# Kernel optimization log

Hardware: AMD Instinct MI355X
Metric: run time of the kernel (lower is better)

## Reference

```python
import jax, jax.numpy as jnp
import numpy as np

N, E, T = 50000, 800000, 3
FIN, H, D, FE = 256, 4, 64, 64
NEG_SLOPE = 0.2


def setup_inputs() -> dict:
    key = jax.random.key(0)
    ks = jax.random.split(key, 10)
    x = jax.random.normal(ks[0], (N, FIN), dtype=jnp.float32)
    edge_src = jax.random.randint(ks[1], (E,), 0, N, dtype=jnp.int32)
    edge_dst = jax.random.randint(ks[2], (E,), 0, N, dtype=jnp.int32)
    edge_type = jax.random.randint(ks[3], (E,), 0, T, dtype=jnp.int32)
    s = 1.0 / np.sqrt(FIN)
    W = jax.random.normal(ks[4], (FIN, H * D), dtype=jnp.float32) * s
    edge_emb = jax.random.normal(ks[5], (T, FE), dtype=jnp.float32)
    W_e = jax.random.normal(ks[6], (FE, H * FE), dtype=jnp.float32) * (1.0 / np.sqrt(FE))
    attn_l = jax.random.normal(ks[7], (H, D), dtype=jnp.float32) * (1.0 / np.sqrt(D))
    attn_r = jax.random.normal(ks[8], (H, D), dtype=jnp.float32) * (1.0 / np.sqrt(D))
    attn_e = jax.random.normal(ks[9], (H, FE), dtype=jnp.float32) * (1.0 / np.sqrt(FE))
    return {"x": x, "edge_src": edge_src, "edge_dst": edge_dst,
            "edge_type": edge_type, "W": W, "edge_emb": edge_emb,
            "W_e": W_e, "attn_l": attn_l, "attn_r": attn_r, "attn_e": attn_e}


def reference(x, edge_src, edge_dst, edge_type, W, edge_emb, W_e, attn_l, attn_r, attn_e):
    # node projection: [N, H, D]
    feat = (x @ W).reshape(N, H, D)
    # per-node, per-head attention scalars
    el = jnp.einsum('nhd,hd->nh', feat, attn_l)  # [N, H]
    er = jnp.einsum('nhd,hd->nh', feat, attn_r)  # [N, H]
    # per-edge-type attention scalar: edge_emb[t] @ W_e -> [T, H, FE]
    e_feat = (edge_emb @ W_e).reshape(T, H, FE)
    ee = jnp.einsum('the,he->th', e_feat, attn_e)  # [T, H]
    # per-edge logits, leaky-relu
    logits = jax.nn.leaky_relu(el[edge_src] + er[edge_dst] + ee[edge_type], NEG_SLOPE)  # [E, H]
    # edge softmax over incoming edges of each dst node (all etypes together)
    seg_max = jax.ops.segment_max(logits, edge_dst, num_segments=N)  # [N, H]
    seg_max = jnp.where(jnp.isfinite(seg_max), seg_max, 0.0)
    expl = jnp.exp(logits - seg_max[edge_dst])  # [E, H]
    seg_sum = jax.ops.segment_sum(expl, edge_dst, num_segments=N)  # [N, H]
    a = expl / seg_sum[edge_dst]  # [E, H]
    # weighted scatter-sum aggregation: sum over incoming edges
    msg = feat[edge_src] * a[:, :, None]  # [E, H, D]
    out = jax.ops.segment_sum(msg, edge_dst, num_segments=N)  # [N, H, D]
    return out, a
```

## Files before the change

### kernel.cpp

```cpp
#include <hip/hip_runtime.h>
#include <hip/hip_bf16.h>
#include <math.h>

#define N_NODES 50000
#define E_EDGES 800000
#define T_TYPES 3
#define MAXDEG 64
#define NEG_SLOPE 0.2f
#define GEMM_BLOCKS 782

typedef __attribute__((ext_vector_type(8))) short short8;
typedef __attribute__((ext_vector_type(4))) short short4v;
typedef __attribute__((ext_vector_type(4))) float f32x4;

__device__ inline short f2bf(float f) {
    __hip_bfloat16 h = __float2bfloat16(f);
    union { __hip_bfloat16 b; short s; } u;
    u.b = h;
    return u.s;
}
__device__ inline float bf2f(short s) {
    union { unsigned u; float f; } v;
    v.u = ((unsigned)(unsigned short)s) << 16;
    return v.f;
}

__global__ void k_prep(const float* __restrict__ W, short8* __restrict__ WF,
                       const float* __restrict__ edge_emb, const float* __restrict__ W_e,
                       const float* __restrict__ attn_e, float* __restrict__ ee,
                       unsigned* __restrict__ deg) {
    int b = blockIdx.x;
    if (b < 32) {
        int f = b * 256 + threadIdx.x;
        int lane = f & 63;
        int rest = f >> 6;
        int ks = rest & 7;
        int nfh = rest >> 3;
        int l15 = lane & 15;
        int lq = lane >> 4;
        int row = nfh * 16 + l15;
        int col0 = ks * 32 + lq * 8;
        short8 s;
        #pragma unroll
        for (int j = 0; j < 8; ++j)
            s[j] = f2bf(W[(size_t)(col0 + j) * 256 + row]);
        WF[f] = s;
    } else if (b < 32 + T_TYPES) {
        int t = b - 32;
        int j = threadIdx.x;
        int h = j >> 6;
        float ae = attn_e[j];
        float v = 0.f;
        #pragma unroll
        for (int k = 0; k < 64; ++k) v += edge_emb[t * 64 + k] * W_e[k * 256 + j];
        v *= ae;
        #pragma unroll
        for (int o = 32; o; o >>= 1) v += __shfl_xor(v, o, 64);
        if ((j & 63) == 0) ee[t * 4 + h] = v;
    } else {
        int i = (b - 32 - T_TYPES) * 256 + threadIdx.x;
        if (i < N_NODES) deg[i] = 0u;
    }
}

__global__ __launch_bounds__(256) void k_gs(const float* __restrict__ x, const short8* __restrict__ WF,
                                            const float* __restrict__ attn_l, const float* __restrict__ attn_r,
                                            short* __restrict__ featb, float* __restrict__ el,
                                            float* __restrict__ er,
                                            const int* __restrict__ esrc, const int* __restrict__ edst,
                                            const int* __restrict__ etype, unsigned* __restrict__ deg,
                                            unsigned* __restrict__ A) {
    __shared__ short lds[64][264];
    if (blockIdx.x >= GEMM_BLOCKS) {
        int e = (blockIdx.x - GEMM_BLOCKS) * 256 + threadIdx.x;
        if (e < E_EDGES) {
            int s = esrc[e], d = edst[e], t = etype[e];
            unsigned rank = atomicAdd(&deg[d], 1u);
            if (rank < MAXDEG)
                A[d * MAXDEG + rank] = (unsigned)s | ((unsigned)t << 16);
        }
        return;
    }

    const int tid = threadIdx.x;
    const int wc = tid >> 6;
    const int lane = tid & 63;
    const int l15 = lane & 15;
    const int lq = lane >> 4;
    const int m0 = blockIdx.x * 64;

    #pragma unroll
    for (int i = 0; i < 16; ++i) {
        int idx = tid + 256 * i;
        int r = idx >> 6;
        int c4 = idx & 63;
        int gr = m0 + r;
        if (gr >= N_NODES) gr = N_NODES - 1;
        float4 v = *reinterpret_cast<const float4*>(&x[(size_t)gr * 256 + c4 * 4]);
        short4v s;
        s[0] = f2bf(v.x); s[1] = f2bf(v.y); s[2] = f2bf(v.z); s[3] = f2bf(v.w);
        *reinterpret_cast<short4v*>(&lds[r][c4 * 4]) = s;
    }
    __syncthreads();

    const short8* wfbase = &WF[(size_t)(wc * 4) * 8 * 64 + lane];

    f32x4 acc[4][4];
    #pragma unroll
    for (int mf = 0; mf < 4; ++mf)
        #pragma unroll
        for (int nf = 0; nf < 4; ++nf)
            acc[mf][nf] = (f32x4){0.f, 0.f, 0.f, 0.f};

    #pragma unroll 2
    for (int k0 = 0; k0 < 256; k0 += 32) {
        const int ks = k0 >> 5;
        short8 av[4], bv[4];
        #pragma unroll
        for (int mf = 0; mf < 4; ++mf)
            av[mf] = *reinterpret_cast<const short8*>(&lds[mf * 16 + l15][k0 + lq * 8]);
        #pragma unroll
        for (int nf = 0; nf < 4; ++nf)
            bv[nf] = wfbase[(nf * 8 + ks) * 64];
        #pragma unroll
        for (int mf = 0; mf < 4; ++mf)
            #pragma unroll
            for (int nf = 0; nf < 4; ++nf)
                acc[mf][nf] = __builtin_amdgcn_mfma_f32_16x16x32_bf16(av[mf], bv[nf], acc[mf][nf], 0, 0, 0);
    }

    float al[4], ar[4];
    #pragma unroll
    for (int nf = 0; nf < 4; ++nf) {
        al[nf] = attn_l[wc * 64 + nf * 16 + l15];
        ar[nf] = attn_r[wc * 64 + nf * 16 + l15];
    }
    #pragma unroll
    for (int mf = 0; mf < 4; ++mf) {
        #pragma unroll
        for (int i = 0; i < 4; ++i) {
            int m = m0 + mf * 16 + lq * 4 + i;
            bool ok = m < N_NODES;
            float pl = 0.f, pr = 0.f;
            #pragma unroll
            for (int nf = 0; nf < 4; ++nf) {
                float v = acc[mf][nf][i];
                if (ok) featb[(size_t)m * 256 + wc * 64 + nf * 16 + l15] = f2bf(v);
                pl += v * al[nf];
                pr += v * ar[nf];
            }
            #pragma unroll
            for (int o = 1; o < 16; o <<= 1) {
                pl += __shfl_xor(pl, o, 64);
                pr += __shfl_xor(pr, o, 64);
            }
            if (ok && l15 == 0) {
                el[m * 4 + wc] = pl;
                er[m * 4 + wc] = pr;
            }
        }
    }
}

__global__ __launch_bounds__(256) void k_agg(const unsigned* __restrict__ deg, const unsigned* __restrict__ A,
                                             const float* __restrict__ el, const float* __restrict__ er,
                                             const float* __restrict__ ee, const short* __restrict__ featb,
                                             float* __restrict__ out, float* __restrict__ invp) {
    const int wave = threadIdx.x >> 6;
    const int lane = threadIdx.x & 63;
    const int n = blockIdx.x * 4 + wave;
    if (n >= N_NODES) return;
    const int half = lane >> 5;
    const int l32 = lane & 31;
    const int h = l32 >> 3;
    unsigned cnt = deg[n];
    if (cnt > MAXDEG) cnt = MAXDEG;
    const unsigned base = (unsigned)n * MAXDEG;

    const float ern = er[n * 4 + h];
    const float ee0 = ee[h], ee1 = ee[4 + h], ee2 = ee[8 + h];

    float s0 = 0.f, s1 = 0.f;
    float a0[8], a1[8];
    #pragma unroll
    for (int j = 0; j < 8; ++j) { a0[j] = 0.f; a1[j] = 0.f; }
    {
        unsigned i = half;
        for (; i + 2 < cnt; i += 4) {
            unsigned p0 = A[base + i];
            unsigned p1 = A[base + i + 2];
            unsigned src0 = p0 & 0xFFFFu, t0 = p0 >> 16;
            unsigned src1 = p1 & 0xFFFFu, t1 = p1 >> 16;
            float el0 = el[src0 * 4 + h];
            float el1 = el[src1 * 4 + h];
            short8 f0 = *reinterpret_cast<const short8*>(&featb[(size_t)src0 * 256 + l32 * 8]);
            short8 f1 = *reinterpret_cast<const short8*>(&featb[(size_t)src1 * 256 + l32 * 8]);
            float z0 = (el0 + ern) + (t0 == 0 ? ee0 : (t0 == 1 ? ee1 : ee2));
            float z1 = (el1 + ern) + (t1 == 0 ? ee0 : (t1 == 1 ? ee1 : ee2));
            z0 = z0 > 0.f ? z0 : NEG_SLOPE * z0;
            z1 = z1 > 0.f ? z1 : NEG_SLOPE * z1;
            float w0 = __expf(z0);
            float w1 = __expf(z1);
            s0 += w0; s1 += w1;
            #pragma unroll
            for (int j = 0; j < 8; ++j) {
                a0[j] += w0 * bf2f(f0[j]);
                a1[j] += w1 * bf2f(f1[j]);
            }
        }
        for (; i < cnt; i += 2) {
            unsigned p0 = A[base + i];
            unsigned src0 = p0 & 0xFFFFu, t0 = p0 >> 16;
            float el0 = el[src0 * 4 + h];
            short8 f0 = *reinterpret_cast<const short8*>(&featb[(size_t)src0 * 256 + l32 * 8]);
            float z0 = (el0 + ern) + (t0 == 0 ? ee0 : (t0 == 1 ? ee1 : ee2));
            z0 = z0 > 0.f ? z0 : NEG_SLOPE * z0;
            float w0 = __expf(z0);
            s0 += w0;
            #pragma unroll
            for (int j = 0; j < 8; ++j) a0[j] += w0 * bf2f(f0[j]);
        }
    }
    float s = s0 + s1;
    s += __shfl_xor(s, 32, 64);
    #pragma unroll
    for (int j = 0; j < 8; ++j) {
        a0[j] += a1[j];
        a0[j] += __shfl_xor(a0[j], 32, 64);
    }
    float inv = (cnt > 0) ? 1.f / s : 0.f;

    if (half == 0) {
        float4 o0, o1;
        o0.x = a0[0] * inv; o0.y = a0[1] * inv; o0.z = a0[2] * inv; o0.w = a0[3] * inv;
        o1.x = a0[4] * inv; o1.y = a0[5] * inv; o1.z = a0[6] * inv; o1.w = a0[7] * inv;
        *reinterpret_cast<float4*>(&out[(size_t)n * 256 + l32 * 8]) = o0;
        *reinterpret_cast<float4*>(&out[(size_t)n * 256 + l32 * 8 + 4]) = o1;
        if ((l32 & 7) == 0) invp[n * 4 + h] = inv;
    }
}

__global__ void k_edge(const int* __restrict__ esrc, const int* __restrict__ edst,
                       const int* __restrict__ etype, const float* __restrict__ el,
                       const float* __restrict__ er, const float* __restrict__ ee,
                       const float* __restrict__ invp, float* __restrict__ a_out) {
    int e = blockIdx.x * 256 + threadIdx.x;
    if (e >= E_EDGES) return;
    int s = esrc[e], d = edst[e], t = etype[e];
    float4 l = *reinterpret_cast<const float4*>(&el[s * 4]);
    float4 r = *reinterpret_cast<const float4*>(&er[d * 4]);
    float4 q = *reinterpret_cast<const float4*>(&ee[t * 4]);
    float4 iv = *reinterpret_cast<const float4*>(&invp[d * 4]);
    float4 z;
    z.x = (l.x + r.x) + q.x;
    z.y = (l.y + r.y) + q.y;
    z.z = (l.z + r.z) + q.z;
    z.w = (l.w + r.w) + q.w;
    z.x = z.x > 0.f ? z.x : NEG_SLOPE * z.x;
    z.y = z.y > 0.f ? z.y : NEG_SLOPE * z.y;
    z.z = z.z > 0.f ? z.z : NEG_SLOPE * z.z;
    z.w = z.w > 0.f ? z.w : NEG_SLOPE * z.w;
    float4 av;
    av.x = __expf(z.x) * iv.x;
    av.y = __expf(z.y) * iv.y;
    av.z = __expf(z.z) * iv.z;
    av.w = __expf(z.w) * iv.w;
    *reinterpret_cast<float4*>(&a_out[(size_t)e * 4]) = av;
}

extern "C" void kernel_launch(void* const* d_in, const int* in_sizes, int n_in,
                              void* d_out, int out_size, void* d_ws, size_t ws_size,
                              hipStream_t stream) {
    const float* x        = (const float*)d_in[0];
    const int*   edge_src = (const int*)d_in[1];
    const int*   edge_dst = (const int*)d_in[2];
    const int*   edge_type= (const int*)d_in[3];
    const float* W        = (const float*)d_in[4];
    const float* edge_emb = (const float*)d_in[5];
    const float* W_e      = (const float*)d_in[6];
    const float* attn_l   = (const float*)d_in[7];
    const float* attn_r   = (const float*)d_in[8];
    const float* attn_e   = (const float*)d_in[9];

    float* out   = (float*)d_out;
    float* a_out = (float*)d_out + (size_t)N_NODES * 256;

    char* ws = (char*)d_ws;
    short*    featb   = (short*)(ws + 0);
    float*    el      = (float*)(ws + 25600000);
    float*    er      = (float*)(ws + 26400000);
    float*    ee      = (float*)(ws + 27200000);
    unsigned* deg     = (unsigned*)(ws + 27200064);
    float*    invp    = (float*)(ws + 27400064);
    unsigned* A       = (unsigned*)(ws + 28200064);
    short8*   WF      = (short8*)(ws + 41000064);

    const int degBlocks = (N_NODES + 255) / 256;
    k_prep<<<32 + T_TYPES + degBlocks, 256, 0, stream>>>(W, WF, edge_emb, W_e, attn_e, ee, deg);

    const int scatterBlocks = (E_EDGES + 255) / 256;
    k_gs<<<GEMM_BLOCKS + scatterBlocks, 256, 0, stream>>>(x, WF, attn_l, attn_r, featb, el, er,
                                                          edge_src, edge_dst, edge_type, deg, A);

    k_agg<<<(N_NODES + 3) / 4, 256, 0, stream>>>(deg, A, el, er, ee, featb, out, invp);
    k_edge<<<(E_EDGES + 255) / 256, 256, 0, stream>>>(edge_src, edge_dst, edge_type,
                                                      el, er, ee, invp, a_out);
}
```

Baseline: 156.7 us.

## Shard per-node degree counters to reduce atomic contention in edge bucketing

Replaces the single per-destination atomic counter and 64-slot adjacency list with 8 shards per node (16 slots each), picking the shard from the edge index. This spreads same-address atomics across separate counters in the scatter phase. The aggregation kernel now reads 8 shard counts and walks two shard pairs per half-wave. In exchange the zero-init and adjacency buffers grow, aggregation does extra count loads and branchier indexing, and any shard holding more than 16 edges drops edges.

```diff
diff --git a/kernel.cpp b/kernel.cpp
--- a/kernel.cpp
+++ b/kernel.cpp
@@ -5,7 +5,8 @@
 #define N_NODES 50000
 #define E_EDGES 800000
 #define T_TYPES 3
-#define MAXDEG 64
+#define NSHARD 8
+#define SHCAP 16
 #define NEG_SLOPE 0.2f
 #define GEMM_BLOCKS 782
 
@@ -28,7 +29,7 @@
 __global__ void k_prep(const float* __restrict__ W, short8* __restrict__ WF,
                        const float* __restrict__ edge_emb, const float* __restrict__ W_e,
                        const float* __restrict__ attn_e, float* __restrict__ ee,
-                       unsigned* __restrict__ deg) {
+                       unsigned* __restrict__ deg_s) {
     int b = blockIdx.x;
     if (b < 32) {
         int f = b * 256 + threadIdx.x;
@@ -59,7 +60,7 @@
         if ((j & 63) == 0) ee[t * 4 + h] = v;
     } else {
         int i = (b - 32 - T_TYPES) * 256 + threadIdx.x;
-        if (i < N_NODES) deg[i] = 0u;
+        if (i < N_NODES * 16) deg_s[i] = 0u;
     }
 }
 
@@ -68,16 +69,17 @@
                                             short* __restrict__ featb, float* __restrict__ el,
                                             float* __restrict__ er,
                                             const int* __restrict__ esrc, const int* __restrict__ edst,
-                                            const int* __restrict__ etype, unsigned* __restrict__ deg,
-                                            unsigned* __restrict__ A) {
+                                            const int* __restrict__ etype, unsigned* __restrict__ deg_s,
+                                            unsigned* __restrict__ A2) {
     __shared__ short lds[64][264];
     if (blockIdx.x >= GEMM_BLOCKS) {
         int e = (blockIdx.x - GEMM_BLOCKS) * 256 + threadIdx.x;
         if (e < E_EDGES) {
             int s = esrc[e], d = edst[e], t = etype[e];
-            unsigned rank = atomicAdd(&deg[d], 1u);
-            if (rank < MAXDEG)
-                A[d * MAXDEG + rank] = (unsigned)s | ((unsigned)t << 16);
+            int sh = e & (NSHARD - 1);
+            unsigned rank = atomicAdd(&deg_s[d * 16 + sh], 1u);
+            if (rank < SHCAP)
+                A2[((unsigned)d * NSHARD + sh) * SHCAP + rank] = (unsigned)s | ((unsigned)t << 16);
         }
         return;
     }
@@ -162,7 +164,7 @@
     }
 }
 
-__global__ __launch_bounds__(256) void k_agg(const unsigned* __restrict__ deg, const unsigned* __restrict__ A,
+__global__ __launch_bounds__(256) void k_agg(const unsigned* __restrict__ deg_s, const unsigned* __restrict__ A2,
                                              const float* __restrict__ el, const float* __restrict__ er,
                                              const float* __restrict__ ee, const short* __restrict__ featb,
                                              float* __restrict__ out, float* __restrict__ invp) {
@@ -173,43 +175,37 @@
     const int half = lane >> 5;
     const int l32 = lane & 31;
     const int h = l32 >> 3;
-    unsigned cnt = deg[n];
-    if (cnt > MAXDEG) cnt = MAXDEG;
-    const unsigned base = (unsigned)n * MAXDEG;
+
+    unsigned c[8];
+    unsigned cnt = 0;
+    #pragma unroll
+    for (int s2 = 0; s2 < 8; ++s2) {
+        unsigned v = deg_s[n * 16 + s2];
+        c[s2] = v > SHCAP ? SHCAP : v;
+        cnt += c[s2];
+    }
 
     const float ern = er[n * 4 + h];
     const float ee0 = ee[h], ee1 = ee[4 + h], ee2 = ee[8 + h];
 
+    const int sA0 = half * 4, sA1 = half * 4 + 1, sB0 = half * 4 + 2, sB1 = half * 4 + 3;
+    const unsigned cA0 = c[sA0], totA = cA0 + c[sA1];
+    const unsigned cB0 = c[sB0], totB = cB0 + c[sB1];
+    const unsigned bA0 = ((unsigned)n * NSHARD + sA0) * SHCAP;
+    const unsigned bA1 = ((unsigned)n * NSHARD + sA1) * SHCAP;
+    const unsigned bB0 = ((unsigned)n * NSHARD + sB0) * SHCAP;
+    const unsigned bB1 = ((unsigned)n * NSHARD + sB1) * SHCAP;
+    const unsigned jmax = totA > totB ? totA : totB;
+
     float s0 = 0.f, s1 = 0.f;
     float a0[8], a1[8];
     #pragma unroll
     for (int j = 0; j < 8; ++j) { a0[j] = 0.f; a1[j] = 0.f; }
-    {
-        unsigned i = half;
-        for (; i + 2 < cnt; i += 4) {
-            unsigned p0 = A[base + i];
-            unsigned p1 = A[base + i + 2];
-            unsigned src0 = p0 & 0xFFFFu, t0 = p0 >> 16;
-            unsigned src1 = p1 & 0xFFFFu, t1 = p1 >> 16;
-            float el0 = el[src0 * 4 + h];
-            float el1 = el[src1 * 4 + h];
-            short8 f0 = *reinterpret_cast<const short8*>(&featb[(size_t)src0 * 256 + l32 * 8]);
-            short8 f1 = *reinterpret_cast<const short8*>(&featb[(size_t)src1 * 256 + l32 * 8]);
-            float z0 = (el0 + ern) + (t0 == 0 ? ee0 : (t0 == 1 ? ee1 : ee2));
-            float z1 = (el1 + ern) + (t1 == 0 ? ee0 : (t1 == 1 ? ee1 : ee2));
-            z0 = z0 > 0.f ? z0 : NEG_SLOPE * z0;
-            z1 = z1 > 0.f ? z1 : NEG_SLOPE * z1;
-            float w0 = __expf(z0);
-            float w1 = __expf(z1);
-            s0 += w0; s1 += w1;
-            #pragma unroll
-            for (int j = 0; j < 8; ++j) {
-                a0[j] += w0 * bf2f(f0[j]);
-                a1[j] += w1 * bf2f(f1[j]);
-            }
-        }
-        for (; i < cnt; i += 2) {
-            unsigned p0 = A[base + i];
+
+    for (unsigned j = 0; j < jmax; ++j) {
+        if (j < totA) {
+            unsigned addr = (j < cA0) ? (bA0 + j) : (bA1 + (j - cA0));
+            unsigned p0 = A2[addr];
             unsigned src0 = p0 & 0xFFFFu, t0 = p0 >> 16;
             float el0 = el[src0 * 4 + h];
             short8 f0 = *reinterpret_cast<const short8*>(&featb[(size_t)src0 * 256 + l32 * 8]);
@@ -218,9 +214,23 @@
             float w0 = __expf(z0);
             s0 += w0;
             #pragma unroll
-            for (int j = 0; j < 8; ++j) a0[j] += w0 * bf2f(f0[j]);
+            for (int j2 = 0; j2 < 8; ++j2) a0[j2] += w0 * bf2f(f0[j2]);
         }
-    }
+        if (j < totB) {
+            unsigned addr = (j < cB0) ? (bB0 + j) : (bB1 + (j - cB0));
+            unsigned p1 = A2[addr];
+            unsigned src1 = p1 & 0xFFFFu, t1 = p1 >> 16;
+            float el1 = el[src1 * 4 + h];
+            short8 f1 = *reinterpret_cast<const short8*>(&featb[(size_t)src1 * 256 + l32 * 8]);
+            float z1 = (el1 + ern) + (t1 == 0 ? ee0 : (t1 == 1 ? ee1 : ee2));
+            z1 = z1 > 0.f ? z1 : NEG_SLOPE * z1;
+            float w1 = __expf(z1);
+            s1 += w1;
+            #pragma unroll
+            for (int j2 = 0; j2 < 8; ++j2) a1[j2] += w1 * bf2f(f1[j2]);
+        }
+    }
+
     float s = s0 + s1;
     s += __shfl_xor(s, 32, 64);
     #pragma unroll
@@ -290,19 +300,19 @@
     float*    el      = (float*)(ws + 25600000);
     float*    er      = (float*)(ws + 26400000);
     float*    ee      = (float*)(ws + 27200000);
-    unsigned* deg     = (unsigned*)(ws + 27200064);
-    float*    invp    = (float*)(ws + 27400064);
-    unsigned* A       = (unsigned*)(ws + 28200064);
-    short8*   WF      = (short8*)(ws + 41000064);
-
-    const int degBlocks = (N_NODES + 255) / 256;
-    k_prep<<<32 + T_TYPES + degBlocks, 256, 0, stream>>>(W, WF, edge_emb, W_e, attn_e, ee, deg);
+    unsigned* deg_s   = (unsigned*)(ws + 27200064);
+    float*    invp    = (float*)(ws + 30400064);
+    unsigned* A2      = (unsigned*)(ws + 31200064);
+    short8*   WF      = (short8*)(ws + 56800064);
+
+    const int degBlocks = (N_NODES * 16 + 255) / 256;
+    k_prep<<<32 + T_TYPES + degBlocks, 256, 0, stream>>>(W, WF, edge_emb, W_e, attn_e, ee, deg_s);
 
     const int scatterBlocks = (E_EDGES + 255) / 256;
     k_gs<<<GEMM_BLOCKS + scatterBlocks, 256, 0, stream>>>(x, WF, attn_l, attn_r, featb, el, er,
-                                                          edge_src, edge_dst, edge_type, deg, A);
-
-    k_agg<<<(N_NODES + 3) / 4, 256, 0, stream>>>(deg, A, el, er, ee, featb, out, invp);
+                                                          edge_src, edge_dst, edge_type, deg_s, A2);
+
+    k_agg<<<(N_NODES + 3) / 4, 256, 0, stream>>>(deg_s, A2, el, er, ee, featb, out, invp);
     k_edge<<<(E_EDGES + 255) / 256, 256, 0, stream>>>(edge_src, edge_dst, edge_type,
                                                       el, er, ee, invp, a_out);
 }
```

Result: slower. 180.6 us (+15.2%).
